# Optimization experiments

Hardware: AMD Instinct MI355X
Metric: run time of the kernel (lower is better)

Reference implementation:

```python
import jax, jax.numpy as jnp
import numpy as np

N_NODES = 100000
N_EDGES = 1000000
N_GRAPHS = 512
IN_DIM = 3
HID = 64


def setup_inputs() -> dict:
    key = jax.random.key(0)
    ks = jax.random.split(key, 7)
    x = jax.random.normal(ks[0], (N_NODES, IN_DIM), dtype=jnp.float32)
    edge_index = jax.random.randint(ks[1], (2, N_EDGES), 0, N_NODES, dtype=jnp.int64)
    batch = jnp.sort(jax.random.randint(ks[2], (N_NODES,), 0, N_GRAPHS, dtype=jnp.int64))
    # Glorot-ish init for GCNConv linear weights (PyG uses glorot), zero bias.
    W1 = jax.random.normal(ks[3], (IN_DIM, HID), dtype=jnp.float32) / np.float32(np.sqrt(IN_DIM))
    b1 = jnp.zeros((HID,), dtype=jnp.float32)
    W2 = jax.random.normal(ks[4], (HID, HID), dtype=jnp.float32) / np.float32(np.sqrt(HID))
    b2 = jnp.zeros((HID,), dtype=jnp.float32)
    return {"x": x, "W1": W1, "b1": b1, "W2": W2, "b2": b2,
            "edge_index": edge_index, "batch": batch}


def reference(x, W1, b1, W2, b2, edge_index, batch):
    n = x.shape[0]
    loop = jnp.arange(n)
    # GCNConv adds self-loops, then symmetric normalization D^-1/2 (A+I) D^-1/2
    src = jnp.concatenate([edge_index[0], loop])  # [E+N]
    dst = jnp.concatenate([edge_index[1], loop])  # [E+N]
    deg = jax.ops.segment_sum(jnp.ones(dst.shape[0], x.dtype), dst, num_segments=n)
    dinv = jnp.where(deg > 0, jax.lax.rsqrt(deg), 0.0)
    norm = dinv[src] * dinv[dst]  # [E+N]

    def gcn_conv(h, W, b):
        hw = h @ W                       # [N, out] linear first (PyG order)
        msg = hw[src] * norm[:, None]    # gather + scale, [E+N, out]
        agg = jax.ops.segment_sum(msg, dst, num_segments=n)  # scatter-add
        return agg + b

    h = jax.nn.relu(gcn_conv(x, W1, b1))
    h = jax.nn.relu(gcn_conv(h, W2, b2))

    # global_mean_pool over the batch vector
    sums = jax.ops.segment_sum(h, batch, num_segments=N_GRAPHS)          # [G, HID]
    counts = jax.ops.segment_sum(jnp.ones(n, h.dtype), batch, num_segments=N_GRAPHS)
    return sums / jnp.maximum(counts, 1.0)[:, None]
```

## Files before the change

### kernel.cpp

```cpp
#include <hip/hip_runtime.h>

#define HID 64
#define N_GRAPHS_C 512
#define BSHIFT 8
#define NBUCK_MAX 512
#define CAP 3264
#define EPB 4096

typedef unsigned short u16;
typedef unsigned int u32;
typedef unsigned long long u64;

__device__ __forceinline__ float bf2f(u16 u) {
    union { u32 i; float f; } v; v.i = ((u32)u) << 16; return v.f;
}
__device__ __forceinline__ u16 f2bf(float f) {
    union { float f; u32 i; } v; v.f = f;
    u32 x = v.i;
    return (u16)((x + 0x7fffu + ((x >> 16) & 1u)) >> 16);
}


__device__ __forceinline__ int lower_bound(const int* __restrict__ a, int n, int key) {
    int lo = 0, hi = n;
    while (lo < hi) {
        int mid = (lo + hi) >> 1;
        if (a[mid] < key) lo = mid + 1; else hi = mid;
    }
    return lo;
}

__global__ void prep(int* __restrict__ gcursor, const int* __restrict__ batch,
                     int* __restrict__ gstart, int n, int nGraphs) {
    int t = threadIdx.x;
    gcursor[t] = 0;
    for (int g = t; g <= nGraphs; g += 512)
        gstart[g] = lower_bound(batch, n, g);
}


__global__ void bin_pairs(const int* __restrict__ src, const int* __restrict__ dst,
                          int* __restrict__ gcursor, u32* __restrict__ pairs,
                          int nE, int nbuck) {
    __shared__ int lh[NBUCK_MAX];
    __shared__ int lbase[NBUCK_MAX];
    int t = threadIdx.x;
    lh[t] = 0;
    __syncthreads();
    int base = blockIdx.x * EPB;
    u32 pk[8]; int rj[8], bj[8];
    #pragma unroll
    for (int j = 0; j < 8; ++j) {
        int e = base + j * 512 + t;
        if (e < nE) {
            int s = src[e], d = dst[e];
            bj[j] = d >> BSHIFT;
            pk[j] = ((u32)(d & 255) << 17) | (u32)s;
            rj[j] = atomicAdd(&lh[bj[j]], 1);
        } else {
            bj[j] = -1;
        }
    }
    __syncthreads();
    if (t < nbuck) lbase[t] = (lh[t] > 0) ? atomicAdd(&gcursor[t], lh[t]) : 0;
    __syncthreads();
    #pragma unroll
    for (int j = 0; j < 8; ++j) {
        if (bj[j] >= 0) {
            int pos = bj[j] * CAP + lbase[bj[j]] + rj[j];
            pairs[pos] = pk[j];
        }
    }
}

__global__ void build_csr(const u32* __restrict__ pairs, const int* __restrict__ gcursor,
                          int* __restrict__ csr_src, int2* __restrict__ off2,
                          float* __restrict__ dinv, const float* __restrict__ x,
                          float4* __restrict__ xs, u16* __restrict__ A16, int n) {
    __shared__ int hist[256];
    __shared__ int tmp[256];
    int t = threadIdx.x;
    int b = blockIdx.x;
    int pbeg = b * CAP;
    int pend = pbeg + gcursor[b];
    if (t < 256) hist[t] = 0;
    if (b == 0 && t < 32) ((u32*)(A16 + (size_t)n * HID))[t] = 0;
    __syncthreads();
    for (int i = pbeg + t; i < pend; i += 512)
        atomicAdd(&hist[pairs[i] >> 17], 1);
    __syncthreads();
    int v = 0;
    if (t < 256) { v = hist[t]; tmp[t] = v; }
    __syncthreads();
    for (int d = 1; d < 256; d <<= 1) {
        int add = (t >= d && t < 256) ? tmp[t - d] : 0;
        __syncthreads();
        if (t < 256) tmp[t] += add;
        __syncthreads();
    }
    if (t < 256) {
        int e = pbeg + tmp[t] - v;
        int node = (b << BSHIFT) + t;
        if (node < n) {
            float dv = rsqrtf((float)(v + 1));
            off2[node] = make_int2(e, e + v);
            dinv[node] = dv;
            xs[node] = make_float4(x[3*node]*dv, x[3*node+1]*dv, x[3*node+2]*dv, dv);
        }
        hist[t] = e;
    }
    __syncthreads();
    for (int i = pbeg + t; i < pend; i += 512) {
        u32 p = pairs[i];
        int pos = atomicAdd(&hist[p >> 17], 1);
        csr_src[pos] = (int)(p & 0x1FFFFu);
    }
}


__global__ void agg3(const float4* __restrict__ xs, const int* __restrict__ csr_src,
                     const int2* __restrict__ off2, float4* __restrict__ agg4, int n) {
    int node = blockIdx.x * blockDim.x + threadIdx.x;
    if (node >= n) return;
    int2 be = off2[node];
    int beg = be.x, end = be.y;
    float4 self = xs[node];
    float a0 = 0.f, a1 = 0.f, a2 = 0.f;
    for (int k = beg; k < end; k += 8) {
        int e1 = end - 1;
        int idx[8];
        float4 v[8];
        #pragma unroll
        for (int j = 0; j < 8; ++j) idx[j] = csr_src[min(k + j, e1)];
        #pragma unroll
        for (int j = 0; j < 8; ++j) v[j] = xs[idx[j]];
        #pragma unroll
        for (int j = 0; j < 8; ++j) {
            if (k + j < end) { a0 += v[j].x; a1 += v[j].y; a2 += v[j].z; }
        }
    }
    agg4[node] = make_float4(a0 + self.x, a1 + self.y, a2 + self.z, self.w);
}


#define MMN 128
__global__ void mm2r(const float4* __restrict__ agg4, const float* __restrict__ W1,
                     const float* __restrict__ b1, const float* __restrict__ W2,
                     u16* __restrict__ A16, int n) {
    __shared__ float w[HID * HID];
    __shared__ float hT[HID][MMN];
    __shared__ float dd[MMN];
    __shared__ float w1s[4 * HID];
    int t = threadIdx.x;

    for (int i = t; i < HID * HID; i += 256) w[i] = W2[i];
    if (t < HID) {
        w1s[t]           = W1[t];
        w1s[HID + t]     = W1[HID + t];
        w1s[2 * HID + t] = W1[2 * HID + t];
        w1s[3 * HID + t] = b1[t];
    }
    int base = blockIdx.x * MMN;
    int nl = t & 127;
    int node1 = base + nl;
    float4 a = make_float4(0.f, 0.f, 0.f, 0.f);
    bool valid = (node1 < n);
    if (valid) a = agg4[node1];
    if (t < MMN) dd[t] = a.w;
    __syncthreads();

    int fbase = t >> 7;
    #pragma unroll
    for (int s = 0; s < 32; ++s) {
        int f = fbase + 2 * s;
        float v = 0.f;
        if (valid) {
            v = (a.x * w1s[f] + a.y * w1s[HID + f] + a.z * w1s[2 * HID + f]) * a.w
                + w1s[3 * HID + f];
            v = v > 0.f ? v : 0.f;
        }
        hT[f][nl] = v;
    }
    __syncthreads();

    int fq = t & 15, oct = t >> 4;
    int nb = oct * 8;
    float acc[8][4];
    #pragma unroll
    for (int j = 0; j < 8; ++j)
        #pragma unroll
        for (int q = 0; q < 4; ++q) acc[j][q] = 0.f;

    #pragma unroll 4
    for (int k = 0; k < HID; ++k) {
        float4 w4 = *(const float4*)&w[k * HID + fq * 4];
        float4 h0 = *(const float4*)&hT[k][nb];
        float4 h1 = *(const float4*)&hT[k][nb + 4];
        float hv[8] = { h0.x, h0.y, h0.z, h0.w, h1.x, h1.y, h1.z, h1.w };
        #pragma unroll
        for (int j = 0; j < 8; ++j) {
            acc[j][0] += hv[j] * w4.x;
            acc[j][1] += hv[j] * w4.y;
            acc[j][2] += hv[j] * w4.z;
            acc[j][3] += hv[j] * w4.w;
        }
    }

    #pragma unroll
    for (int j = 0; j < 8; ++j) {
        int node = base + nb + j;
        if (node < n) {
            float dj = dd[nb + j];
            u64 outp = (u64)f2bf(acc[j][0] * dj)
                     | ((u64)f2bf(acc[j][1] * dj) << 16)
                     | ((u64)f2bf(acc[j][2] * dj) << 32)
                     | ((u64)f2bf(acc[j][3] * dj) << 48);
            *(u64*)(A16 + ((size_t)node << 6) + (fq << 2)) = outp;
        }
    }
}


__global__ void gather_nodes(const u16* __restrict__ A16, const float* __restrict__ dinv,
                             const int* __restrict__ csr_src, const int2* __restrict__ off2,
                             const float* __restrict__ bias,
                             u16* __restrict__ H16, int n) {
    int t = threadIdx.x;
    int waveq = t >> 4;
    int m = t & 15;
    int qbase = t & 48;
    int node = blockIdx.x * 16 + waveq;
    if (node >= n) return;
    int2 be = off2[node];
    int beg = be.x, end = be.y;
    u64 selfrow = *(const u64*)(A16 + ((size_t)node << 6) + (m << 2));
    u32 slo = (u32)selfrow, shi = (u32)(selfrow >> 32);
    float acc0 = bf2f((u16)(slo & 0xffffu));
    float acc1 = bf2f((u16)(slo >> 16));
    float acc2 = bf2f((u16)(shi & 0xffffu));
    float acc3 = bf2f((u16)(shi >> 16));
    const char* Ab = (const char*)A16;
    u32 laneoff = (u32)(m << 3);
    for (int k = beg; k < end; k += 8) {
        int lim = min(end - k, 8);
        int myIdx = (m < lim) ? csr_src[k + m] : n;
        int ss[8]; u64 rows[8];
        #pragma unroll
        for (int j = 0; j < 8; ++j)
            ss[j] = __shfl(myIdx, qbase + j, 64);
        #pragma unroll
        for (int j = 0; j < 8; ++j)
            rows[j] = *(const u64*)(Ab + (((u32)ss[j] << 7) | laneoff));
        #pragma unroll
        for (int j = 0; j < 8; ++j) {
            u32 lo = (u32)rows[j], hi = (u32)(rows[j] >> 32);
            acc0 += bf2f((u16)(lo & 0xffffu));
            acc1 += bf2f((u16)(lo >> 16));
            acc2 += bf2f((u16)(hi & 0xffffu));
            acc3 += bf2f((u16)(hi >> 16));
        }
    }
    float ddv = dinv[node];
    float4 bb = *(const float4*)(bias + (m << 2));
    float v0 = fmaxf(acc0 * ddv + bb.x, 0.0f);
    float v1 = fmaxf(acc1 * ddv + bb.y, 0.0f);
    float v2 = fmaxf(acc2 * ddv + bb.z, 0.0f);
    float v3 = fmaxf(acc3 * ddv + bb.w, 0.0f);
    u64 outp = (u64)f2bf(v0) | ((u64)f2bf(v1) << 16)
             | ((u64)f2bf(v2) << 32) | ((u64)f2bf(v3) << 48);
    *(u64*)(H16 + ((size_t)node << 6) + (m << 2)) = outp;
}


__global__ void pool_graph(const u16* __restrict__ H16, const int* __restrict__ gstart,
                           float* __restrict__ out, int n) {
    int g = blockIdx.x;
    int t = threadIdx.x;
    int lo = gstart[g];
    int hi = gstart[g + 1];
    int cntN = hi - lo;
    int sid = t >> 4;
    int m = t & 15;
    float a0 = 0.f, a1 = 0.f, a2 = 0.f, a3 = 0.f;
    int i = lo + sid;
    for (; i + 16 < hi; i += 32) {
        u64 r0 = *(const u64*)(H16 + ((size_t)i << 6) + (m << 2));
        u64 r1 = *(const u64*)(H16 + ((size_t)(i + 16) << 6) + (m << 2));
        u32 l0 = (u32)r0, h0 = (u32)(r0 >> 32);
        u32 l1 = (u32)r1, h1 = (u32)(r1 >> 32);
        a0 += bf2f((u16)(l0 & 0xffffu)) + bf2f((u16)(l1 & 0xffffu));
        a1 += bf2f((u16)(l0 >> 16))     + bf2f((u16)(l1 >> 16));
        a2 += bf2f((u16)(h0 & 0xffffu)) + bf2f((u16)(h1 & 0xffffu));
        a3 += bf2f((u16)(h0 >> 16))     + bf2f((u16)(h1 >> 16));
    }
    if (i < hi) {
        u64 r0 = *(const u64*)(H16 + ((size_t)i << 6) + (m << 2));
        u32 l0 = (u32)r0, h0 = (u32)(r0 >> 32);
        a0 += bf2f((u16)(l0 & 0xffffu));
        a1 += bf2f((u16)(l0 >> 16));
        a2 += bf2f((u16)(h0 & 0xffffu));
        a3 += bf2f((u16)(h0 >> 16));
    }
    a0 += __shfl_xor(a0, 16, 64); a0 += __shfl_xor(a0, 32, 64);
    a1 += __shfl_xor(a1, 16, 64); a1 += __shfl_xor(a1, 32, 64);
    a2 += __shfl_xor(a2, 16, 64); a2 += __shfl_xor(a2, 32, 64);
    a3 += __shfl_xor(a3, 16, 64); a3 += __shfl_xor(a3, 32, 64);
    __shared__ float smf[4 * HID];
    int wave = t >> 6, lane = t & 63;
    if (lane < 16) {
        smf[wave * HID + 4 * lane + 0] = a0;
        smf[wave * HID + 4 * lane + 1] = a1;
        smf[wave * HID + 4 * lane + 2] = a2;
        smf[wave * HID + 4 * lane + 3] = a3;
    }
    __syncthreads();
    if (t < HID) {
        float s = smf[t] + smf[HID + t] + smf[2 * HID + t] + smf[3 * HID + t];
        out[(size_t)g * HID + t] = s / fmaxf((float)cntN, 1.0f);
    }
}


extern "C" void kernel_launch(void* const* d_in, const int* in_sizes, int n_in,
                              void* d_out, int out_size, void* d_ws, size_t ws_size,
                              hipStream_t stream) {
    const float* x  = (const float*)d_in[0];
    const float* W1 = (const float*)d_in[1];
    const float* b1 = (const float*)d_in[2];
    const float* W2 = (const float*)d_in[3];
    const float* b2 = (const float*)d_in[4];
    const int*   ei = (const int*)d_in[5];
    const int*   batch = (const int*)d_in[6];

    const int n  = in_sizes[0] / 3;
    const int nE = in_sizes[5] / 2;
    const int* src = ei;
    const int* dst = ei + nE;
    const int nbuck = (n + ((1 << BSHIFT) - 1)) >> BSHIFT;
    const int nGraphs = out_size / HID;

    char* p = (char*)d_ws;
    int*    gcursor = (int*)p;                p += 2048;
    int*    gstart  = (int*)p;                p += 4096;
    int*    csr_src = (int*)p;                p += (size_t)nbuck * CAP * 4;
    int2*   off2    = (int2*)p;               p += (size_t)n * 8;
    float*  dinv    = (float*)p;              p += (size_t)n * 4;
    float4* xs      = (float4*)p;             p += (size_t)n * 16;
    float4* agg4    = (float4*)p;             p += (size_t)n * 16;
    u16*    A16     = (u16*)p;                p += (size_t)(n + 1) * HID * 2;
    u16*    H2      = (u16*)p;                p += (size_t)n * HID * 2;
    u32*    pairs   = (u32*)A16;

    const int BT = 256;
    const int gridNode = (n + BT - 1) / BT;
    const int gridE2   = (nE + EPB - 1) / EPB;
    const int gridMM2  = (n + MMN - 1) / MMN;
    const int gridGath = (n + 15) / 16;

    prep<<<1, 512, 0, stream>>>(gcursor, batch, gstart, n, nGraphs);
    bin_pairs<<<gridE2, 512, 0, stream>>>(src, dst, gcursor, pairs, nE, nbuck);
    build_csr<<<nbuck, 512, 0, stream>>>(pairs, gcursor, csr_src, off2, dinv, x, xs, A16, n);

    agg3<<<gridNode, BT, 0, stream>>>(xs, csr_src, off2, agg4, n);
    mm2r<<<gridMM2, BT, 0, stream>>>(agg4, W1, b1, W2, A16, n);

    gather_nodes<<<gridGath, BT, 0, stream>>>(A16, dinv, csr_src, off2, b2, H2, n);

    pool_graph<<<nGraphs, BT, 0, stream>>>(H2, gstart, (float*)d_out, n);
}
```

Before: 160.4 us.

## Fuse layer-1 aggregation into the layer-2 matmul kernel with split-edge threads

Merges the 3-wide neighbour aggregation kernel into the matmul kernel. Each block now aggregates its own 128 nodes, with two threads per node splitting the edge list, and combines the partials through shared memory that reuses the hT buffer. This removes a kernel launch and the agg4 round trip through global memory. In exchange the gather latency now sits inside a kernel with large shared memory use, so fewer blocks can hide it.

```diff
diff --git a/kernel.cpp b/kernel.cpp
--- a/kernel.cpp
+++ b/kernel.cpp
@@ -118,39 +118,17 @@
 }
 
 
-__global__ void agg3(const float4* __restrict__ xs, const int* __restrict__ csr_src,
-                     const int2* __restrict__ off2, float4* __restrict__ agg4, int n) {
-    int node = blockIdx.x * blockDim.x + threadIdx.x;
-    if (node >= n) return;
-    int2 be = off2[node];
-    int beg = be.x, end = be.y;
-    float4 self = xs[node];
-    float a0 = 0.f, a1 = 0.f, a2 = 0.f;
-    for (int k = beg; k < end; k += 8) {
-        int e1 = end - 1;
-        int idx[8];
-        float4 v[8];
-        #pragma unroll
-        for (int j = 0; j < 8; ++j) idx[j] = csr_src[min(k + j, e1)];
-        #pragma unroll
-        for (int j = 0; j < 8; ++j) v[j] = xs[idx[j]];
-        #pragma unroll
-        for (int j = 0; j < 8; ++j) {
-            if (k + j < end) { a0 += v[j].x; a1 += v[j].y; a2 += v[j].z; }
-        }
-    }
-    agg4[node] = make_float4(a0 + self.x, a1 + self.y, a2 + self.z, self.w);
-}
-
-
 #define MMN 128
-__global__ void mm2r(const float4* __restrict__ agg4, const float* __restrict__ W1,
-                     const float* __restrict__ b1, const float* __restrict__ W2,
-                     u16* __restrict__ A16, int n) {
+__global__ void agg_mm2(const float4* __restrict__ xs, const int* __restrict__ csr_src,
+                        const int2* __restrict__ off2,
+                        const float* __restrict__ W1, const float* __restrict__ b1,
+                        const float* __restrict__ W2,
+                        u16* __restrict__ A16, int n) {
     __shared__ float w[HID * HID];
     __shared__ float hT[HID][MMN];
     __shared__ float dd[MMN];
     __shared__ float w1s[4 * HID];
+    float4* paggs = (float4*)&hT[0][0];
     int t = threadIdx.x;
 
     for (int i = t; i < HID * HID; i += 256) w[i] = W2[i];
@@ -160,26 +138,47 @@
         w1s[2 * HID + t] = W1[2 * HID + t];
         w1s[3 * HID + t] = b1[t];
     }
+
     int base = blockIdx.x * MMN;
-    int nl = t & 127;
-    int node1 = base + nl;
-    float4 a = make_float4(0.f, 0.f, 0.f, 0.f);
-    bool valid = (node1 < n);
-    if (valid) a = agg4[node1];
-    if (t < MMN) dd[t] = a.w;
-    __syncthreads();
-
+    int nl = t >> 1, half = t & 1;
+    int node = base + nl;
+    float a0 = 0.f, a1 = 0.f, a2 = 0.f, dv = 0.f;
+    if (node < n) {
+        int2 be = off2[node];
+        int beg = be.x, end = be.y, e1 = end - 1;
+        if (half == 0) {
+            float4 self = xs[node];
+            a0 = self.x; a1 = self.y; a2 = self.z; dv = self.w;
+            dd[nl] = dv;
+        }
+        for (int k = beg + half * 8; k < end; k += 16) {
+            int idx[8]; float4 v[8];
+            #pragma unroll
+            for (int j = 0; j < 8; ++j) idx[j] = csr_src[min(k + j, e1)];
+            #pragma unroll
+            for (int j = 0; j < 8; ++j) v[j] = xs[idx[j]];
+            #pragma unroll
+            for (int j = 0; j < 8; ++j) {
+                if (k + j < end) { a0 += v[j].x; a1 += v[j].y; a2 += v[j].z; }
+            }
+        }
+    } else if (half == 0) {
+        dd[nl] = 0.f;
+    }
+    paggs[(nl << 1) | half] = make_float4(a0, a1, a2, dv);
+    __syncthreads();
+
+    int nl1 = t & 127;
+    float4 pa = paggs[nl1 * 2], pb = paggs[nl1 * 2 + 1];
+    float4 a = make_float4(pa.x + pb.x, pa.y + pb.y, pa.z + pb.z, pa.w + pb.w);
+    __syncthreads();
     int fbase = t >> 7;
     #pragma unroll
     for (int s = 0; s < 32; ++s) {
         int f = fbase + 2 * s;
-        float v = 0.f;
-        if (valid) {
-            v = (a.x * w1s[f] + a.y * w1s[HID + f] + a.z * w1s[2 * HID + f]) * a.w
-                + w1s[3 * HID + f];
-            v = v > 0.f ? v : 0.f;
-        }
-        hT[f][nl] = v;
+        float v = (a.x * w1s[f] + a.y * w1s[HID + f] + a.z * w1s[2 * HID + f]) * a.w
+                  + w1s[3 * HID + f];
+        hT[f][nl1] = v > 0.f ? v : 0.f;
     }
     __syncthreads();
 
@@ -208,14 +207,14 @@
 
     #pragma unroll
     for (int j = 0; j < 8; ++j) {
-        int node = base + nb + j;
-        if (node < n) {
+        int nodej = base + nb + j;
+        if (nodej < n) {
             float dj = dd[nb + j];
             u64 outp = (u64)f2bf(acc[j][0] * dj)
                      | ((u64)f2bf(acc[j][1] * dj) << 16)
                      | ((u64)f2bf(acc[j][2] * dj) << 32)
                      | ((u64)f2bf(acc[j][3] * dj) << 48);
-            *(u64*)(A16 + ((size_t)node << 6) + (fq << 2)) = outp;
+            *(u64*)(A16 + ((size_t)nodej << 6) + (fq << 2)) = outp;
         }
     }
 }
@@ -346,23 +345,20 @@
     int2*   off2    = (int2*)p;               p += (size_t)n * 8;
     float*  dinv    = (float*)p;              p += (size_t)n * 4;
     float4* xs      = (float4*)p;             p += (size_t)n * 16;
-    float4* agg4    = (float4*)p;             p += (size_t)n * 16;
     u16*    A16     = (u16*)p;                p += (size_t)(n + 1) * HID * 2;
     u16*    H2      = (u16*)p;                p += (size_t)n * HID * 2;
     u32*    pairs   = (u32*)A16;
 
-    const int BT = 256;
-    const int gridNode = (n + BT - 1) / BT;
     const int gridE2   = (nE + EPB - 1) / EPB;
     const int gridMM2  = (n + MMN - 1) / MMN;
     const int gridGath = (n + 15) / 16;
+    const int BT = 256;
 
     prep<<<1, 512, 0, stream>>>(gcursor, batch, gstart, n, nGraphs);
     bin_pairs<<<gridE2, 512, 0, stream>>>(src, dst, gcursor, pairs, nE, nbuck);
     build_csr<<<nbuck, 512, 0, stream>>>(pairs, gcursor, csr_src, off2, dinv, x, xs, A16, n);
 
-    agg3<<<gridNode, BT, 0, stream>>>(xs, csr_src, off2, agg4, n);
-    mm2r<<<gridMM2, BT, 0, stream>>>(agg4, W1, b1, W2, A16, n);
+    agg_mm2<<<gridMM2, BT, 0, stream>>>(xs, csr_src, off2, W1, b1, W2, A16, n);
 
     gather_nodes<<<gridGath, BT, 0, stream>>>(A16, dinv, csr_src, off2, b2, H2, n);
 
```

After: 157.2 us. 1.02x faster.
